# Performance work log

Measured on AMD Instinct MI355X. Metric: run time of the kernel, lower is better.

## Reference

```python
import jax, jax.numpy as jnp
import numpy as np

B, L, P, A = 32, 512, 128, 128   # batch, prot seq len, prot dim, atom dim
N = 1024                          # total atoms (32 per molecule)
H1, H2 = 512, 256                 # hidden_list


def setup_inputs() -> dict:
    key = jax.random.key(0)
    ks = jax.random.split(key, 12)
    atom_embed = jax.random.normal(ks[0], (N, A), dtype=jnp.float32)
    protSeq_embed = jax.random.normal(ks[1], (B, L, P), dtype=jnp.float32)
    # sorted segment ids, every segment non-empty (32 atoms per molecule)
    atom_splits = jnp.repeat(jnp.arange(B, dtype=jnp.int64), N // B)
    s = 0.05
    att1_W = jax.random.normal(ks[2], (P + A, 128), dtype=jnp.float32) * s
    att1_b = jnp.zeros((128,), dtype=jnp.float32)
    att2_W = jax.random.normal(ks[3], (128, 1), dtype=jnp.float32) * s
    att2_b = jnp.zeros((1,), dtype=jnp.float32)
    d1_W = jax.random.normal(ks[4], (A + P, H1), dtype=jnp.float32) * s
    d1_b = jnp.zeros((H1,), dtype=jnp.float32)
    d2_W = jax.random.normal(ks[5], (H1, H2), dtype=jnp.float32) * s
    d2_b = jnp.zeros((H2,), dtype=jnp.float32)
    out_W = jax.random.normal(ks[6], (H2, 1), dtype=jnp.float32) * s
    out_b = jnp.zeros((1,), dtype=jnp.float32)
    return {"atom_embed": atom_embed, "protSeq_embed": protSeq_embed,
            "atom_splits": atom_splits,
            "att1_W": att1_W, "att1_b": att1_b, "att2_W": att2_W, "att2_b": att2_b,
            "d1_W": d1_W, "d1_b": d1_b, "d2_W": d2_W, "d2_b": d2_b,
            "out_W": out_W, "out_b": out_b}


def reference(atom_embed, protSeq_embed, atom_splits,
              att1_W, att1_b, att2_W, att2_b,
              d1_W, d1_b, d2_W, d2_b, out_W, out_b):
    num_seg = protSeq_embed.shape[0]
    # gather protein rows per atom: [N, L, P]
    prot_g = protSeq_embed[atom_splits]
    # concat with broadcast atom embed: [N, L, P+A]
    atom_x = jnp.broadcast_to(atom_embed[:, None, :], prot_g.shape[:2] + atom_embed.shape[-1:])
    concat = jnp.concatenate([prot_g, atom_x], axis=-1)
    # attention MLP -> scores W: [N, L]
    hid = jnp.tanh(concat @ att1_W + att1_b)
    W = 5.0 * jnp.tanh(hid @ att2_W + att2_b)[..., 0]
    # atom-side weights: exp(max over seq), normalized per segment
    Wc = jnp.exp(jnp.max(W, axis=-1, keepdims=True))                     # [N, 1]
    Sc = jax.ops.segment_sum(Wc, atom_splits, num_segments=num_seg)[atom_splits]
    aa = Wc / Sc                                                          # [N, 1]
    atom_pool = jax.ops.segment_sum(aa * atom_embed, atom_splits, num_segments=num_seg)  # [B, A]
    # protein-side: segment-max scores, softmax over seq, weighted sum
    Wp = jax.ops.segment_max(W, atom_splits, num_segments=num_seg)       # [B, L]
    ap = jax.nn.softmax(Wp, axis=-1)
    prot_pool = jnp.einsum('bl,bld->bd', ap, protSeq_embed)              # [B, P]
    z = jnp.concatenate([atom_pool, prot_pool], axis=-1)
    z = jax.nn.relu(z @ d1_W + d1_b)
    z = jax.nn.relu(z @ d2_W + d2_b)
    return z @ out_W + out_b                                             # [B, 1]
```

## Files before the change

### kernel.cpp

```cpp
#include <hip/hip_runtime.h>
#include <math.h>

#define NATOMS 1024
#define BSEG   32
#define LSEQ   512

__device__ __forceinline__ float fast_tanh(float x) {
    x = fminf(fmaxf(x, -20.0f), 20.0f);
    float e = __expf(2.0f * x);
    return __fdividef(e - 1.0f, e + 1.0f);
}

__global__ __launch_bounds__(256) void row_gemm128_exp(
    const float* __restrict__ X, const float* __restrict__ Wm,
    const float* __restrict__ bias, float* __restrict__ out, int has_bias)
{
    __shared__ float x_s[16][128];
    const int tid = threadIdx.x;
    const long base = (long)blockIdx.x * 16 * 128;
    #pragma unroll
    for (int t = 0; t < 8; ++t) {
        int idx = tid + 256 * t;
        x_s[idx >> 7][idx & 127] = X[base + idx];
    }
    __syncthreads();
    const int j = tid & 127, h = tid >> 7;
    float bv = has_bias ? bias[j] : 0.0f;
    float acc[8];
    #pragma unroll
    for (int i = 0; i < 8; ++i) acc[i] = bv;
    #pragma unroll 4
    for (int k = 0; k < 128; ++k) {
        float w = Wm[k * 128 + j];
        #pragma unroll
        for (int i = 0; i < 8; ++i) acc[i] += x_s[h * 8 + i][k] * w;
    }
    #pragma unroll
    for (int i = 0; i < 8; ++i) {
        float v = fminf(fmaxf(acc[i], -20.0f), 20.0f);
        out[base + (h * 8 + i) * 128 + j] = __expf(2.0f * v);
    }
}

__global__ __launch_bounds__(256) void score2_kernel(
    const float* __restrict__ ep, const float* __restrict__ eb,
    const float* __restrict__ att2_W, const float* __restrict__ att2_b,
    float* __restrict__ Wp, float* __restrict__ pmax)
{
    __shared__ float eps[16 * 128];
    __shared__ float ebs[32 * 132];
    __shared__ float c_s[128];
    __shared__ float pm_s[8 * 33];
    __shared__ float w2sum_s;
    const int tid = threadIdx.x;
    const int chunk = blockIdx.x, b = blockIdx.y;
    const int lbase = chunk * 16;

    #pragma unroll
    for (int t = 0; t < 8; ++t) {
        int idx = tid + 256 * t;
        eps[idx] = ep[((long)b * LSEQ + lbase) * 128 + idx];
    }
    #pragma unroll
    for (int t = 0; t < 16; ++t) {
        int idx = tid + 256 * t;
        int n = idx >> 7, j = idx & 127;
        ebs[n * 132 + j] = eb[(b * 32 + n) * 128 + j];
    }
    if (tid < 128) c_s[tid] = -2.0f * att2_W[tid];
    __syncthreads();
    if (tid < 64) {
        float s = c_s[tid] + c_s[tid + 64];
        #pragma unroll
        for (int m = 32; m; m >>= 1) s += __shfl_xor(s, m);
        if (tid == 0) w2sum_s = -0.5f * s;
    }
    const float b2 = att2_b[0];
    __syncthreads();

    const int n = tid & 31, lg = tid >> 5;
    const float* ebrow = &ebs[n * 132];
    const float* ep0 = &eps[lg * 128];
    const float* ep1 = &eps[(lg + 8) * 128];
    float acc0 = 0.0f, acc1 = 0.0f;
    #pragma unroll 4
    for (int jj = 0; jj < 128; jj += 4) {
        float4 bv = *(const float4*)(ebrow + jj);
        float4 e0 = *(const float4*)(ep0 + jj);
        float4 e1 = *(const float4*)(ep1 + jj);
        float4 cv = *(const float4*)(c_s + jj);
        acc0 += cv.x * __builtin_amdgcn_rcpf(1.0f + e0.x * bv.x);
        acc1 += cv.x * __builtin_amdgcn_rcpf(1.0f + e1.x * bv.x);
        acc0 += cv.y * __builtin_amdgcn_rcpf(1.0f + e0.y * bv.y);
        acc1 += cv.y * __builtin_amdgcn_rcpf(1.0f + e1.y * bv.y);
        acc0 += cv.z * __builtin_amdgcn_rcpf(1.0f + e0.z * bv.z);
        acc1 += cv.z * __builtin_amdgcn_rcpf(1.0f + e1.z * bv.z);
        acc0 += cv.w * __builtin_amdgcn_rcpf(1.0f + e0.w * bv.w);
        acc1 += cv.w * __builtin_amdgcn_rcpf(1.0f + e1.w * bv.w);
    }
    const float base = w2sum_s + b2;
    float W0 = 5.0f * fast_tanh(acc0 + base);
    float W1 = 5.0f * fast_tanh(acc1 + base);

    float m0 = W0, m1 = W1;
    #pragma unroll
    for (int m = 16; m; m >>= 1) {
        m0 = fmaxf(m0, __shfl_xor(m0, m));
        m1 = fmaxf(m1, __shfl_xor(m1, m));
    }
    if (n == 0) {
        Wp[b * LSEQ + lbase + lg] = m0;
        Wp[b * LSEQ + lbase + lg + 8] = m1;
    }
    pm_s[lg * 33 + n] = fmaxf(W0, W1);
    __syncthreads();
    if (tid < 32) {
        float m = pm_s[tid];
        #pragma unroll
        for (int g = 1; g < 8; ++g) m = fmaxf(m, pm_s[g * 33 + tid]);
        pmax[b * 1024 + chunk * 32 + tid] = m;
    }
}

__global__ __launch_bounds__(256) void finish_kernel(
    const float* __restrict__ pmax, const float* __restrict__ Wp,
    const float* __restrict__ atom_embed, const float* __restrict__ out_b,
    float* __restrict__ ap, float* __restrict__ z, float* __restrict__ out)
{
    __shared__ float pm_s[8 * 33];
    __shared__ float expw_s[32];
    __shared__ float red[256];
    __shared__ float sinv_s;
    const int tid = threadIdx.x, b = blockIdx.x;

    {
        int n = tid & 31, cg = tid >> 5;
        float m = -1e30f;
        #pragma unroll
        for (int i = 0; i < 4; ++i)
            m = fmaxf(m, pmax[b * 1024 + (cg * 4 + i) * 32 + n]);
        pm_s[cg * 33 + n] = m;
    }
    __syncthreads();
    if (tid < 32) {
        float m = pm_s[tid];
        #pragma unroll
        for (int g = 1; g < 8; ++g) m = fmaxf(m, pm_s[g * 33 + tid]);
        expw_s[tid] = __expf(m);
    }
    __syncthreads();
    if (tid == 0) {
        float s = 0.0f;
        #pragma unroll
        for (int i = 0; i < 32; ++i) s += expw_s[i];
        sinv_s = 1.0f / s;
        out[b] = out_b[0];
    }
    __syncthreads();
    if (tid < 128) {
        float acc = 0.0f;
        #pragma unroll 4
        for (int nn = 0; nn < 32; ++nn)
            acc += expw_s[nn] * atom_embed[(b * 32 + nn) * 128 + tid];
        z[b * 256 + tid] = acc * sinv_s;
    } else {
        z[b * 256 + tid] = 0.0f;
    }
    float w0 = Wp[b * 512 + tid], w1 = Wp[b * 512 + 256 + tid];
    red[tid] = fmaxf(w0, w1);
    __syncthreads();
    for (int s = 128; s; s >>= 1) {
        if (tid < s) red[tid] = fmaxf(red[tid], red[tid + s]);
        __syncthreads();
    }
    float M = red[0];
    __syncthreads();
    float e0 = __expf(w0 - M), e1 = __expf(w1 - M);
    red[tid] = e0 + e1;
    __syncthreads();
    for (int s = 128; s; s >>= 1) {
        if (tid < s) red[tid] += red[tid + s];
        __syncthreads();
    }
    float Sinv = 1.0f / red[0];
    ap[b * 512 + tid] = e0 * Sinv;
    ap[b * 512 + 256 + tid] = e1 * Sinv;
}

__global__ __launch_bounds__(128) void prot_pool_kernel(
    const float* __restrict__ ap, const float* __restrict__ protSeq,
    float* __restrict__ z)
{
    __shared__ float ap_s[64];
    const int tid = threadIdx.x;
    const int l0 = blockIdx.x * 64, b = blockIdx.y;
    if (tid < 64) ap_s[tid] = ap[b * 512 + l0 + tid];
    __syncthreads();
    float acc = 0.0f;
    #pragma unroll 8
    for (int i = 0; i < 64; ++i)
        acc += ap_s[i] * protSeq[((long)(b * 512 + l0 + i)) * 128 + tid];
    atomicAdd(&z[b * 256 + 128 + tid], acc);
}

__global__ __launch_bounds__(256) void mlp1_kernel(
    const float* __restrict__ z, const float* __restrict__ d1_W,
    const float* __restrict__ d1_b, float* __restrict__ h1)
{
    __shared__ float zs[256];
    __shared__ float part[4 * 65];
    const int tid = threadIdx.x;
    const int c0 = blockIdx.x * 64, b = blockIdx.y;
    zs[tid] = z[b * 256 + tid];
    __syncthreads();
    const int ci = tid & 63, kg = tid >> 6;
    float acc = 0.0f;
    #pragma unroll 8
    for (int k = kg * 64; k < kg * 64 + 64; ++k)
        acc += zs[k] * d1_W[k * 512 + c0 + ci];
    part[kg * 65 + ci] = acc;
    __syncthreads();
    if (tid < 64) {
        float s = part[tid] + part[65 + tid] + part[130 + tid] + part[195 + tid]
                + d1_b[c0 + tid];
        h1[b * 512 + c0 + tid] = fmaxf(s, 0.0f);
    }
}

__global__ __launch_bounds__(256) void mlp2_kernel(
    const float* __restrict__ h1, const float* __restrict__ d2_W,
    const float* __restrict__ d2_b, const float* __restrict__ out_W,
    float* __restrict__ out)
{
    __shared__ float hs[512];
    __shared__ float part[8 * 33];
    const int tid = threadIdx.x;
    const int c0 = blockIdx.x * 32, b = blockIdx.y;
    hs[tid] = h1[b * 512 + tid];
    hs[tid + 256] = h1[b * 512 + 256 + tid];
    __syncthreads();
    const int ci = tid & 31, kg = tid >> 5;
    float acc = 0.0f;
    #pragma unroll 8
    for (int k = kg * 64; k < kg * 64 + 64; ++k)
        acc += hs[k] * d2_W[k * 256 + c0 + ci];
    part[kg * 33 + ci] = acc;
    __syncthreads();
    if (tid < 32) {
        float s = d2_b[c0 + tid];
        #pragma unroll
        for (int g = 0; g < 8; ++g) s += part[g * 33 + tid];
        float contrib = fmaxf(s, 0.0f) * out_W[c0 + tid];
        #pragma unroll
        for (int m = 16; m; m >>= 1) contrib += __shfl_xor(contrib, m);
        if (tid == 0) atomicAdd(&out[b], contrib);
    }
}

extern "C" void kernel_launch(void* const* d_in, const int* in_sizes, int n_in,
                              void* d_out, int out_size, void* d_ws, size_t ws_size,
                              hipStream_t stream) {
    const float* atom_embed = (const float*)d_in[0];
    const float* protSeq    = (const float*)d_in[1];
    const float* att1_W = (const float*)d_in[3];
    const float* att1_b = (const float*)d_in[4];
    const float* att2_W = (const float*)d_in[5];
    const float* att2_b = (const float*)d_in[6];
    const float* d1_W   = (const float*)d_in[7];
    const float* d1_b   = (const float*)d_in[8];
    const float* d2_W   = (const float*)d_in[9];
    const float* d2_b   = (const float*)d_in[10];
    const float* out_W  = (const float*)d_in[11];
    const float* out_b  = (const float*)d_in[12];
    float* out = (float*)d_out;

    float* ws = (float*)d_ws;
    float* ep   = ws;
    float* eb   = ep + 2097152;
    float* Wp   = eb + 131072;
    float* pmax = Wp + 16384;
    float* ap   = pmax + 32768;
    float* z    = ap + 16384;
    float* h1   = z + 8192;

    row_gemm128_exp<<<NATOMS / 16, 256, 0, stream>>>(atom_embed, att1_W + 128 * 128,
                                                     nullptr, eb, 0);
    row_gemm128_exp<<<(BSEG * LSEQ) / 16, 256, 0, stream>>>(protSeq, att1_W,
                                                            att1_b, ep, 1);
    score2_kernel<<<dim3(LSEQ / 16, BSEG), 256, 0, stream>>>(ep, eb, att2_W,
                                                             att2_b, Wp, pmax);
    finish_kernel<<<BSEG, 256, 0, stream>>>(pmax, Wp, atom_embed, out_b, ap, z, out);
    prot_pool_kernel<<<dim3(8, BSEG), 128, 0, stream>>>(ap, protSeq, z);
    mlp1_kernel<<<dim3(8, BSEG), 256, 0, stream>>>(z, d1_W, d1_b, h1);
    mlp2_kernel<<<dim3(8, BSEG), 256, 0, stream>>>(h1, d2_W, d2_b, out_W, out);
}
```

Before: 141.5 us.

## Merge att1 GEMMs into register-tiled kernel and fold softmax normalization into MLP

Result: faster. 128.9 us (-9.0%).

```diff
diff --git a/kernel.cpp b/kernel.cpp
--- a/kernel.cpp
+++ b/kernel.cpp
@@ -11,41 +11,81 @@
     return __fdividef(e - 1.0f, e + 1.0f);
 }
 
-__global__ __launch_bounds__(256) void row_gemm128_exp(
-    const float* __restrict__ X, const float* __restrict__ Wm,
-    const float* __restrict__ bias, float* __restrict__ out, int has_bias)
-{
-    __shared__ float x_s[16][128];
-    const int tid = threadIdx.x;
-    const long base = (long)blockIdx.x * 16 * 128;
-    #pragma unroll
-    for (int t = 0; t < 8; ++t) {
-        int idx = tid + 256 * t;
-        x_s[idx >> 7][idx & 127] = X[base + idx];
-    }
-    __syncthreads();
-    const int j = tid & 127, h = tid >> 7;
-    float bv = has_bias ? bias[j] : 0.0f;
-    float acc[8];
-    #pragma unroll
-    for (int i = 0; i < 8; ++i) acc[i] = bv;
-    #pragma unroll 4
-    for (int k = 0; k < 128; ++k) {
-        float w = Wm[k * 128 + j];
-        #pragma unroll
-        for (int i = 0; i < 8; ++i) acc[i] += x_s[h * 8 + i][k] * w;
-    }
-    #pragma unroll
-    for (int i = 0; i < 8; ++i) {
-        float v = fminf(fmaxf(acc[i], -20.0f), 20.0f);
-        out[base + (h * 8 + i) * 128 + j] = __expf(2.0f * v);
+__global__ __launch_bounds__(256) void gemm_exp_kernel(
+    const float* __restrict__ protSeq, const float* __restrict__ atom_embed,
+    const float* __restrict__ att1_W, const float* __restrict__ att1_b,
+    float* __restrict__ ep, float* __restrict__ eb)
+{
+    __shared__ float xT[64 * 68];
+    __shared__ float ws[64 * 68];
+    const int tid = threadIdx.x;
+    const int bx = blockIdx.x;
+
+    const float* Xb; const float* Wb; const float* bb; float* outp;
+    int rt, ct;
+    if (bx < 512) { rt = bx >> 1; ct = bx & 1;
+        Xb = protSeq + (long)rt * 64 * 128; Wb = att1_W; bb = att1_b;
+        outp = ep + (long)rt * 64 * 128;
+    } else { int e = bx - 512; rt = e >> 1; ct = e & 1;
+        Xb = atom_embed + (long)rt * 64 * 128; Wb = att1_W + 128 * 128; bb = nullptr;
+        outp = eb + (long)rt * 64 * 128;
+    }
+    const int c0 = ct * 64;
+    const int tx = tid & 15, ty = tid >> 4;
+
+    float acc[4][4];
+    #pragma unroll
+    for (int i = 0; i < 4; ++i)
+        #pragma unroll
+        for (int j = 0; j < 4; ++j) acc[i][j] = 0.0f;
+
+    #pragma unroll
+    for (int half = 0; half < 2; ++half) {
+        if (half) __syncthreads();
+        #pragma unroll
+        for (int i = 0; i < 16; ++i) {
+            int idx = tid + 256 * i;
+            int r = idx >> 6, kk = idx & 63;
+            xT[kk * 68 + r] = Xb[r * 128 + half * 64 + kk];
+        }
+        #pragma unroll
+        for (int i = 0; i < 16; ++i) {
+            int idx = tid + 256 * i;
+            int kk = idx >> 6, c = idx & 63;
+            ws[kk * 68 + c] = Wb[(half * 64 + kk) * 128 + c0 + c];
+        }
+        __syncthreads();
+        #pragma unroll 8
+        for (int kk = 0; kk < 64; ++kk) {
+            float4 a = *(const float4*)&xT[kk * 68 + 4 * ty];
+            float4 b = *(const float4*)&ws[kk * 68 + 4 * tx];
+            acc[0][0] += a.x * b.x; acc[0][1] += a.x * b.y;
+            acc[0][2] += a.x * b.z; acc[0][3] += a.x * b.w;
+            acc[1][0] += a.y * b.x; acc[1][1] += a.y * b.y;
+            acc[1][2] += a.y * b.z; acc[1][3] += a.y * b.w;
+            acc[2][0] += a.z * b.x; acc[2][1] += a.z * b.y;
+            acc[2][2] += a.z * b.z; acc[2][3] += a.z * b.w;
+            acc[3][0] += a.w * b.x; acc[3][1] += a.w * b.y;
+            acc[3][2] += a.w * b.z; acc[3][3] += a.w * b.w;
+        }
+    }
+    float4 bias4 = make_float4(0.f, 0.f, 0.f, 0.f);
+    if (bb) bias4 = *(const float4*)&bb[c0 + 4 * tx];
+    #pragma unroll
+    for (int i = 0; i < 4; ++i) {
+        float4 v;
+        v.x = __expf(2.0f * fminf(fmaxf(acc[i][0] + bias4.x, -20.0f), 20.0f));
+        v.y = __expf(2.0f * fminf(fmaxf(acc[i][1] + bias4.y, -20.0f), 20.0f));
+        v.z = __expf(2.0f * fminf(fmaxf(acc[i][2] + bias4.z, -20.0f), 20.0f));
+        v.w = __expf(2.0f * fminf(fmaxf(acc[i][3] + bias4.w, -20.0f), 20.0f));
+        *(float4*)&outp[(4 * ty + i) * 128 + c0 + 4 * tx] = v;
     }
 }
 
 __global__ __launch_bounds__(256) void score2_kernel(
     const float* __restrict__ ep, const float* __restrict__ eb,
     const float* __restrict__ att2_W, const float* __restrict__ att2_b,
-    float* __restrict__ Wp, float* __restrict__ pmax)
+    float* __restrict__ Wp, float* __restrict__ pmax, float* __restrict__ zr)
 {
     __shared__ float eps[16 * 128];
     __shared__ float ebs[32 * 132];
@@ -55,6 +95,8 @@
     const int tid = threadIdx.x;
     const int chunk = blockIdx.x, b = blockIdx.y;
     const int lbase = chunk * 16;
+
+    if (chunk == 0 && tid < 128) zr[b * 128 + tid] = 0.0f;
 
     #pragma unroll
     for (int t = 0; t < 8; ++t) {
@@ -122,96 +164,87 @@
     }
 }
 
-__global__ __launch_bounds__(256) void finish_kernel(
-    const float* __restrict__ pmax, const float* __restrict__ Wp,
-    const float* __restrict__ atom_embed, const float* __restrict__ out_b,
-    float* __restrict__ ap, float* __restrict__ z, float* __restrict__ out)
-{
-    __shared__ float pm_s[8 * 33];
-    __shared__ float expw_s[32];
-    __shared__ float red[256];
-    __shared__ float sinv_s;
-    const int tid = threadIdx.x, b = blockIdx.x;
-
-    {
-        int n = tid & 31, cg = tid >> 5;
-        float m = -1e30f;
-        #pragma unroll
-        for (int i = 0; i < 4; ++i)
-            m = fmaxf(m, pmax[b * 1024 + (cg * 4 + i) * 32 + n]);
-        pm_s[cg * 33 + n] = m;
-    }
-    __syncthreads();
-    if (tid < 32) {
-        float m = pm_s[tid];
-        #pragma unroll
-        for (int g = 1; g < 8; ++g) m = fmaxf(m, pm_s[g * 33 + tid]);
-        expw_s[tid] = __expf(m);
-    }
-    __syncthreads();
-    if (tid == 0) {
-        float s = 0.0f;
-        #pragma unroll
-        for (int i = 0; i < 32; ++i) s += expw_s[i];
-        sinv_s = 1.0f / s;
-        out[b] = out_b[0];
-    }
-    __syncthreads();
-    if (tid < 128) {
+__global__ __launch_bounds__(256) void tail_kernel(
+    const float* __restrict__ Wp, const float* __restrict__ pmax,
+    const float* __restrict__ atom_embed, const float* __restrict__ protSeq,
+    const float* __restrict__ out_b,
+    float* __restrict__ za, float* __restrict__ zr, float* __restrict__ dp,
+    float* __restrict__ out)
+{
+    const int tid = threadIdx.x;
+    const int bx = blockIdx.x, b = blockIdx.y;
+    if (bx < 8) {
+        __shared__ float e_s[64];
+        const int l0 = bx * 64;
+        if (tid < 64) e_s[tid] = __expf(Wp[b * 512 + l0 + tid]);
+        __syncthreads();
+        const int d = tid & 127, half = tid >> 7;
         float acc = 0.0f;
-        #pragma unroll 4
-        for (int nn = 0; nn < 32; ++nn)
-            acc += expw_s[nn] * atom_embed[(b * 32 + nn) * 128 + tid];
-        z[b * 256 + tid] = acc * sinv_s;
+        #pragma unroll 8
+        for (int i = 0; i < 32; ++i) {
+            int l = l0 + half * 32 + i;
+            acc += e_s[half * 32 + i] * protSeq[((long)(b * 512 + l)) * 128 + d];
+        }
+        atomicAdd(&zr[b * 128 + d], acc);
     } else {
-        z[b * 256 + tid] = 0.0f;
-    }
-    float w0 = Wp[b * 512 + tid], w1 = Wp[b * 512 + 256 + tid];
-    red[tid] = fmaxf(w0, w1);
-    __syncthreads();
-    for (int s = 128; s; s >>= 1) {
-        if (tid < s) red[tid] = fmaxf(red[tid], red[tid + s]);
-        __syncthreads();
-    }
-    float M = red[0];
-    __syncthreads();
-    float e0 = __expf(w0 - M), e1 = __expf(w1 - M);
-    red[tid] = e0 + e1;
-    __syncthreads();
-    for (int s = 128; s; s >>= 1) {
-        if (tid < s) red[tid] += red[tid + s];
-        __syncthreads();
-    }
-    float Sinv = 1.0f / red[0];
-    ap[b * 512 + tid] = e0 * Sinv;
-    ap[b * 512 + 256 + tid] = e1 * Sinv;
-}
-
-__global__ __launch_bounds__(128) void prot_pool_kernel(
-    const float* __restrict__ ap, const float* __restrict__ protSeq,
-    float* __restrict__ z)
-{
-    __shared__ float ap_s[64];
-    const int tid = threadIdx.x;
-    const int l0 = blockIdx.x * 64, b = blockIdx.y;
-    if (tid < 64) ap_s[tid] = ap[b * 512 + l0 + tid];
-    __syncthreads();
-    float acc = 0.0f;
-    #pragma unroll 8
-    for (int i = 0; i < 64; ++i)
-        acc += ap_s[i] * protSeq[((long)(b * 512 + l0 + i)) * 128 + tid];
-    atomicAdd(&z[b * 256 + 128 + tid], acc);
+        __shared__ float pm_s[8 * 33];
+        __shared__ float expw_s[32];
+        __shared__ float red[256];
+        __shared__ float sinv_s;
+        {
+            int n = tid & 31, cg = tid >> 5;
+            float m = -1e30f;
+            #pragma unroll
+            for (int i = 0; i < 4; ++i)
+                m = fmaxf(m, pmax[b * 1024 + (cg * 4 + i) * 32 + n]);
+            pm_s[cg * 33 + n] = m;
+        }
+        __syncthreads();
+        if (tid < 32) {
+            float m = pm_s[tid];
+            #pragma unroll
+            for (int g = 1; g < 8; ++g) m = fmaxf(m, pm_s[g * 33 + tid]);
+            expw_s[tid] = __expf(m);
+        }
+        __syncthreads();
+        if (tid == 0) {
+            float s = 0.0f;
+            #pragma unroll
+            for (int i = 0; i < 32; ++i) s += expw_s[i];
+            sinv_s = 1.0f / s;
+            out[b] = out_b[0];
+        }
+        __syncthreads();
+        if (tid < 128) {
+            float acc = 0.0f;
+            #pragma unroll 4
+            for (int nn = 0; nn < 32; ++nn)
+                acc += expw_s[nn] * atom_embed[(b * 32 + nn) * 128 + tid];
+            za[b * 128 + tid] = acc * sinv_s;
+        }
+        float e0 = __expf(Wp[b * 512 + tid]);
+        float e1 = __expf(Wp[b * 512 + 256 + tid]);
+        red[tid] = e0 + e1;
+        __syncthreads();
+        for (int s = 128; s; s >>= 1) {
+            if (tid < s) red[tid] += red[tid + s];
+            __syncthreads();
+        }
+        if (tid == 0) dp[b] = red[0];
+    }
 }
 
 __global__ __launch_bounds__(256) void mlp1_kernel(
-    const float* __restrict__ z, const float* __restrict__ d1_W,
+    const float* __restrict__ za, const float* __restrict__ zr,
+    const float* __restrict__ dp, const float* __restrict__ d1_W,
     const float* __restrict__ d1_b, float* __restrict__ h1)
 {
     __shared__ float zs[256];
     __shared__ float part[4 * 65];
     const int tid = threadIdx.x;
     const int c0 = blockIdx.x * 64, b = blockIdx.y;
-    zs[tid] = z[b * 256 + tid];
+    const float rdp = 1.0f / dp[b];
+    zs[tid] = (tid < 128) ? za[b * 128 + tid] : zr[b * 128 + tid - 128] * rdp;
     __syncthreads();
     const int ci = tid & 63, kg = tid >> 6;
     float acc = 0.0f;
@@ -279,18 +312,17 @@
     float* eb   = ep + 2097152;
     float* Wp   = eb + 131072;
     float* pmax = Wp + 16384;
-    float* ap   = pmax + 32768;
-    float* z    = ap + 16384;
-    float* h1   = z + 8192;
-
-    row_gemm128_exp<<<NATOMS / 16, 256, 0, stream>>>(atom_embed, att1_W + 128 * 128,
-                                                     nullptr, eb, 0);
-    row_gemm128_exp<<<(BSEG * LSEQ) / 16, 256, 0, stream>>>(protSeq, att1_W,
-                                                            att1_b, ep, 1);
+    float* za   = pmax + 32768;
+    float* zr   = za + 4096;
+    float* dp   = zr + 4096;
+    float* h1   = dp + 32;
+
+    gemm_exp_kernel<<<544, 256, 0, stream>>>(protSeq, atom_embed, att1_W,
+                                             att1_b, ep, eb);
     score2_kernel<<<dim3(LSEQ / 16, BSEG), 256, 0, stream>>>(ep, eb, att2_W,
-                                                             att2_b, Wp, pmax);
-    finish_kernel<<<BSEG, 256, 0, stream>>>(pmax, Wp, atom_embed, out_b, ap, z, out);
-    prot_pool_kernel<<<dim3(8, BSEG), 128, 0, stream>>>(ap, protSeq, z);
-    mlp1_kernel<<<dim3(8, BSEG), 256, 0, stream>>>(z, d1_W, d1_b, h1);
+                                                             att2_b, Wp, pmax, zr);
+    tail_kernel<<<dim3(9, BSEG), 256, 0, stream>>>(Wp, pmax, atom_embed, protSeq,
+                                                   out_b, za, zr, dp, out);
+    mlp1_kernel<<<dim3(8, BSEG), 256, 0, stream>>>(za, zr, dp, d1_W, d1_b, h1);
     mlp2_kernel<<<dim3(8, BSEG), 256, 0, stream>>>(h1, d2_W, d2_b, out_W, out);
 }
```

## Fuse pipeline into four kernels with register-tiled GEMM and fused softmax pooling

Applied to the files above, without the earlier changes.

Measured after the change: 127.1 us. 1.11x faster.

```diff
diff --git a/kernel.cpp b/kernel.cpp
--- a/kernel.cpp
+++ b/kernel.cpp
@@ -11,209 +11,242 @@
     return __fdividef(e - 1.0f, e + 1.0f);
 }
 
-__global__ __launch_bounds__(256) void row_gemm128_exp(
-    const float* __restrict__ X, const float* __restrict__ Wm,
-    const float* __restrict__ bias, float* __restrict__ out, int has_bias)
+__device__ __forceinline__ float trm(float c, float p, float e) {
+    return c * __builtin_amdgcn_rcpf(fmaf(p, e, 1.0f));
+}
+
+__global__ __launch_bounds__(256) void gemm_exp_kernel(
+    const float* __restrict__ protSeq, const float* __restrict__ atom_embed,
+    const float* __restrict__ att1_W, const float* __restrict__ att1_b,
+    float* __restrict__ ep, float* __restrict__ eb,
+    float* __restrict__ zr, float* __restrict__ dp)
 {
-    __shared__ float x_s[16][128];
-    const int tid = threadIdx.x;
-    const long base = (long)blockIdx.x * 16 * 128;
-    #pragma unroll
-    for (int t = 0; t < 8; ++t) {
-        int idx = tid + 256 * t;
-        x_s[idx >> 7][idx & 127] = X[base + idx];
-    }
-    __syncthreads();
-    const int j = tid & 127, h = tid >> 7;
-    float bv = has_bias ? bias[j] : 0.0f;
-    float acc[8];
-    #pragma unroll
-    for (int i = 0; i < 8; ++i) acc[i] = bv;
-    #pragma unroll 4
-    for (int k = 0; k < 128; ++k) {
-        float w = Wm[k * 128 + j];
-        #pragma unroll
-        for (int i = 0; i < 8; ++i) acc[i] += x_s[h * 8 + i][k] * w;
-    }
-    #pragma unroll
-    for (int i = 0; i < 8; ++i) {
-        float v = fminf(fmaxf(acc[i], -20.0f), 20.0f);
-        out[base + (h * 8 + i) * 128 + j] = __expf(2.0f * v);
-    }
-}
-
-__global__ __launch_bounds__(256) void score2_kernel(
+    __shared__ float xT[64 * 68];
+    __shared__ float wsb[64 * 132];
+    const int tid = threadIdx.x, bx = blockIdx.x;
+
+    const float* Xb; const float* Wb; const float* bb; float* outp;
+    if (bx < 256) {
+        Xb = protSeq + (long)bx * 64 * 128; Wb = att1_W; bb = att1_b;
+        outp = ep + (long)bx * 64 * 128;
+    } else {
+        int e = bx - 256;
+        zr[e * 256 + tid] = 0.0f;
+        if (e == 0 && tid < 32) dp[tid] = 0.0f;
+        Xb = atom_embed + (long)e * 64 * 128; Wb = att1_W + 128 * 128; bb = nullptr;
+        outp = eb + (long)e * 64 * 128;
+    }
+    const int tx = tid & 15, ty = tid >> 4;
+
+    float acc[4][8];
+    #pragma unroll
+    for (int i = 0; i < 4; ++i)
+        #pragma unroll
+        for (int j = 0; j < 8; ++j) acc[i][j] = 0.0f;
+
+    #pragma unroll
+    for (int half = 0; half < 2; ++half) {
+        if (half) __syncthreads();
+        #pragma unroll
+        for (int t = 0; t < 4; ++t) {
+            int flat = (tid + 256 * t) * 4;
+            int r = flat >> 6, kk = flat & 63;
+            float4 v = *(const float4*)&Xb[r * 128 + half * 64 + kk];
+            xT[kk * 68 + r] = v.x; xT[(kk + 1) * 68 + r] = v.y;
+            xT[(kk + 2) * 68 + r] = v.z; xT[(kk + 3) * 68 + r] = v.w;
+        }
+        #pragma unroll
+        for (int t = 0; t < 8; ++t) {
+            int flat = (tid + 256 * t) * 4;
+            int kk = flat >> 7, c = flat & 127;
+            *(float4*)&wsb[kk * 132 + c] = *(const float4*)&Wb[(half * 64 + kk) * 128 + c];
+        }
+        __syncthreads();
+        #pragma unroll 4
+        for (int kk = 0; kk < 64; ++kk) {
+            float4 a  = *(const float4*)&xT[kk * 68 + 4 * ty];
+            float4 w0 = *(const float4*)&wsb[kk * 132 + 8 * tx];
+            float4 w1 = *(const float4*)&wsb[kk * 132 + 8 * tx + 4];
+            #pragma unroll
+            for (int i = 0; i < 4; ++i) {
+                float av = (i == 0) ? a.x : (i == 1) ? a.y : (i == 2) ? a.z : a.w;
+                acc[i][0] += av * w0.x; acc[i][1] += av * w0.y;
+                acc[i][2] += av * w0.z; acc[i][3] += av * w0.w;
+                acc[i][4] += av * w1.x; acc[i][5] += av * w1.y;
+                acc[i][6] += av * w1.z; acc[i][7] += av * w1.w;
+            }
+        }
+    }
+    float bias[8];
+    #pragma unroll
+    for (int j = 0; j < 8; ++j) bias[j] = 0.0f;
+    if (bb) {
+        *(float4*)&bias[0] = *(const float4*)&bb[8 * tx];
+        *(float4*)&bias[4] = *(const float4*)&bb[8 * tx + 4];
+    }
+    #pragma unroll
+    for (int i = 0; i < 4; ++i) {
+        float o[8];
+        #pragma unroll
+        for (int j = 0; j < 8; ++j) {
+            float v = fminf(fmaxf(acc[i][j] + bias[j], -20.0f), 20.0f);
+            o[j] = __expf(2.0f * v);
+        }
+        int row = 4 * ty + i;
+        *(float4*)&outp[row * 128 + 8 * tx]     = make_float4(o[0], o[1], o[2], o[3]);
+        *(float4*)&outp[row * 128 + 8 * tx + 4] = make_float4(o[4], o[5], o[6], o[7]);
+    }
+}
+
+__global__ __launch_bounds__(256) void score3_kernel(
     const float* __restrict__ ep, const float* __restrict__ eb,
     const float* __restrict__ att2_W, const float* __restrict__ att2_b,
-    float* __restrict__ Wp, float* __restrict__ pmax)
+    const float* __restrict__ protSeq,
+    float* __restrict__ pmax, float* __restrict__ zr, float* __restrict__ dp)
 {
-    __shared__ float eps[16 * 128];
+    __shared__ float eps[64 * 132];
     __shared__ float ebs[32 * 132];
     __shared__ float c_s[128];
-    __shared__ float pm_s[8 * 33];
-    __shared__ float w2sum_s;
+    __shared__ float wps[64];
+    __shared__ float es[64];
+    __shared__ float pmn[32 * 33];
+    __shared__ float part[256];
+    __shared__ float base_s;
     const int tid = threadIdx.x;
     const int chunk = blockIdx.x, b = blockIdx.y;
-    const int lbase = chunk * 16;
+    const int lbase = chunk * 64;
 
     #pragma unroll
     for (int t = 0; t < 8; ++t) {
-        int idx = tid + 256 * t;
-        eps[idx] = ep[((long)b * LSEQ + lbase) * 128 + idx];
-    }
-    #pragma unroll
-    for (int t = 0; t < 16; ++t) {
-        int idx = tid + 256 * t;
-        int n = idx >> 7, j = idx & 127;
-        ebs[n * 132 + j] = eb[(b * 32 + n) * 128 + j];
+        int flat = (tid + 256 * t) * 4;
+        int l = flat >> 7, j = flat & 127;
+        *(float4*)&eps[l * 132 + j] =
+            *(const float4*)&ep[((long)(b * 512 + lbase + l)) * 128 + j];
+    }
+    #pragma unroll
+    for (int t = 0; t < 4; ++t) {
+        int flat = (tid + 256 * t) * 4;
+        int n = flat >> 7, j = flat & 127;
+        *(float4*)&ebs[n * 132 + j] = *(const float4*)&eb[(b * 32 + n) * 128 + j];
     }
     if (tid < 128) c_s[tid] = -2.0f * att2_W[tid];
     __syncthreads();
     if (tid < 64) {
         float s = c_s[tid] + c_s[tid + 64];
         #pragma unroll
-        for (int m = 32; m; m >>= 1) s += __shfl_xor(s, m);
-        if (tid == 0) w2sum_s = -0.5f * s;
-    }
-    const float b2 = att2_b[0];
-    __syncthreads();
-
-    const int n = tid & 31, lg = tid >> 5;
-    const float* ebrow = &ebs[n * 132];
-    const float* ep0 = &eps[lg * 128];
-    const float* ep1 = &eps[(lg + 8) * 128];
-    float acc0 = 0.0f, acc1 = 0.0f;
+        for (int m = 1; m < 64; m <<= 1) s += __shfl_xor(s, m);
+        if (tid == 0) base_s = -0.5f * s + att2_b[0];
+    }
+    __syncthreads();
+
+    const int ng = tid & 7, lg = tid >> 3;
+    const float* e0 = &ebs[ng * 132];
+    const float* e1 = &ebs[(ng + 8) * 132];
+    const float* e2 = &ebs[(ng + 16) * 132];
+    const float* e3 = &ebs[(ng + 24) * 132];
+    const float* p0 = &eps[lg * 132];
+    const float* p1 = &eps[(lg + 32) * 132];
+    float a00 = 0, a01 = 0, a10 = 0, a11 = 0, a20 = 0, a21 = 0, a30 = 0, a31 = 0;
+    #pragma unroll 2
+    for (int jj = 0; jj < 128; jj += 4) {
+        float4 c4 = *(const float4*)&c_s[jj];
+        float4 q0 = *(const float4*)(p0 + jj);
+        float4 q1 = *(const float4*)(p1 + jj);
+        float4 b0 = *(const float4*)(e0 + jj);
+        float4 b1 = *(const float4*)(e1 + jj);
+        float4 b2v = *(const float4*)(e2 + jj);
+        float4 b3 = *(const float4*)(e3 + jj);
+#define DOCOMP(C, Q0, Q1, B0, B1, B2, B3) \
+        a00 += trm(C, Q0, B0); a01 += trm(C, Q1, B0); \
+        a10 += trm(C, Q0, B1); a11 += trm(C, Q1, B1); \
+        a20 += trm(C, Q0, B2); a21 += trm(C, Q1, B2); \
+        a30 += trm(C, Q0, B3); a31 += trm(C, Q1, B3);
+        DOCOMP(c4.x, q0.x, q1.x, b0.x, b1.x, b2v.x, b3.x)
+        DOCOMP(c4.y, q0.y, q1.y, b0.y, b1.y, b2v.y, b3.y)
+        DOCOMP(c4.z, q0.z, q1.z, b0.z, b1.z, b2v.z, b3.z)
+        DOCOMP(c4.w, q0.w, q1.w, b0.w, b1.w, b2v.w, b3.w)
+#undef DOCOMP
+    }
+    const float bs = base_s;
+    float W00 = 5.0f * fast_tanh(a00 + bs), W01 = 5.0f * fast_tanh(a01 + bs);
+    float W10 = 5.0f * fast_tanh(a10 + bs), W11 = 5.0f * fast_tanh(a11 + bs);
+    float W20 = 5.0f * fast_tanh(a20 + bs), W21 = 5.0f * fast_tanh(a21 + bs);
+    float W30 = 5.0f * fast_tanh(a30 + bs), W31 = 5.0f * fast_tanh(a31 + bs);
+
+    float m0 = fmaxf(fmaxf(W00, W10), fmaxf(W20, W30));
+    float m1 = fmaxf(fmaxf(W01, W11), fmaxf(W21, W31));
+    #pragma unroll
+    for (int d = 1; d < 8; d <<= 1) {
+        m0 = fmaxf(m0, __shfl_xor(m0, d));
+        m1 = fmaxf(m1, __shfl_xor(m1, d));
+    }
+    if (ng == 0) { wps[lg] = m0; wps[lg + 32] = m1; }
+    pmn[lg * 33 + ng]      = fmaxf(W00, W01);
+    pmn[lg * 33 + ng + 8]  = fmaxf(W10, W11);
+    pmn[lg * 33 + ng + 16] = fmaxf(W20, W21);
+    pmn[lg * 33 + ng + 24] = fmaxf(W30, W31);
+    __syncthreads();
+    if (tid < 32) {
+        float m = pmn[tid];
+        #pragma unroll
+        for (int g = 1; g < 32; ++g) m = fmaxf(m, pmn[g * 33 + tid]);
+        pmax[b * 256 + chunk * 32 + tid] = m;
+    }
+    if (tid < 64) es[tid] = __expf(wps[tid]);
+    __syncthreads();
+    if (tid < 64) {
+        float v = es[tid];
+        #pragma unroll
+        for (int d = 1; d < 64; d <<= 1) v += __shfl_xor(v, d);
+        if (tid == 0) atomicAdd(&dp[b], v);
+    }
+    const int dd = tid & 127, hf = tid >> 7;
+    float az = 0.0f;
     #pragma unroll 4
-    for (int jj = 0; jj < 128; jj += 4) {
-        float4 bv = *(const float4*)(ebrow + jj);
-        float4 e0 = *(const float4*)(ep0 + jj);
-        float4 e1 = *(const float4*)(ep1 + jj);
-        float4 cv = *(const float4*)(c_s + jj);
-        acc0 += cv.x * __builtin_amdgcn_rcpf(1.0f + e0.x * bv.x);
-        acc1 += cv.x * __builtin_amdgcn_rcpf(1.0f + e1.x * bv.x);
-        acc0 += cv.y * __builtin_amdgcn_rcpf(1.0f + e0.y * bv.y);
-        acc1 += cv.y * __builtin_amdgcn_rcpf(1.0f + e1.y * bv.y);
-        acc0 += cv.z * __builtin_amdgcn_rcpf(1.0f + e0.z * bv.z);
-        acc1 += cv.z * __builtin_amdgcn_rcpf(1.0f + e1.z * bv.z);
-        acc0 += cv.w * __builtin_amdgcn_rcpf(1.0f + e0.w * bv.w);
-        acc1 += cv.w * __builtin_amdgcn_rcpf(1.0f + e1.w * bv.w);
-    }
-    const float base = w2sum_s + b2;
-    float W0 = 5.0f * fast_tanh(acc0 + base);
-    float W1 = 5.0f * fast_tanh(acc1 + base);
-
-    float m0 = W0, m1 = W1;
-    #pragma unroll
-    for (int m = 16; m; m >>= 1) {
-        m0 = fmaxf(m0, __shfl_xor(m0, m));
-        m1 = fmaxf(m1, __shfl_xor(m1, m));
-    }
-    if (n == 0) {
-        Wp[b * LSEQ + lbase + lg] = m0;
-        Wp[b * LSEQ + lbase + lg + 8] = m1;
-    }
-    pm_s[lg * 33 + n] = fmaxf(W0, W1);
-    __syncthreads();
-    if (tid < 32) {
-        float m = pm_s[tid];
-        #pragma unroll
-        for (int g = 1; g < 8; ++g) m = fmaxf(m, pm_s[g * 33 + tid]);
-        pmax[b * 1024 + chunk * 32 + tid] = m;
-    }
-}
-
-__global__ __launch_bounds__(256) void finish_kernel(
-    const float* __restrict__ pmax, const float* __restrict__ Wp,
-    const float* __restrict__ atom_embed, const float* __restrict__ out_b,
-    float* __restrict__ ap, float* __restrict__ z, float* __restrict__ out)
-{
-    __shared__ float pm_s[8 * 33];
-    __shared__ float expw_s[32];
-    __shared__ float red[256];
-    __shared__ float sinv_s;
-    const int tid = threadIdx.x, b = blockIdx.x;
-
-    {
-        int n = tid & 31, cg = tid >> 5;
-        float m = -1e30f;
-        #pragma unroll
-        for (int i = 0; i < 4; ++i)
-            m = fmaxf(m, pmax[b * 1024 + (cg * 4 + i) * 32 + n]);
-        pm_s[cg * 33 + n] = m;
-    }
-    __syncthreads();
-    if (tid < 32) {
-        float m = pm_s[tid];
-        #pragma unroll
-        for (int g = 1; g < 8; ++g) m = fmaxf(m, pm_s[g * 33 + tid]);
-        expw_s[tid] = __expf(m);
-    }
-    __syncthreads();
-    if (tid == 0) {
-        float s = 0.0f;
-        #pragma unroll
-        for (int i = 0; i < 32; ++i) s += expw_s[i];
-        sinv_s = 1.0f / s;
-        out[b] = out_b[0];
-    }
-    __syncthreads();
-    if (tid < 128) {
-        float acc = 0.0f;
-        #pragma unroll 4
-        for (int nn = 0; nn < 32; ++nn)
-            acc += expw_s[nn] * atom_embed[(b * 32 + nn) * 128 + tid];
-        z[b * 256 + tid] = acc * sinv_s;
-    } else {
-        z[b * 256 + tid] = 0.0f;
-    }
-    float w0 = Wp[b * 512 + tid], w1 = Wp[b * 512 + 256 + tid];
-    red[tid] = fmaxf(w0, w1);
-    __syncthreads();
-    for (int s = 128; s; s >>= 1) {
-        if (tid < s) red[tid] = fmaxf(red[tid], red[tid + s]);
-        __syncthreads();
-    }
-    float M = red[0];
-    __syncthreads();
-    float e0 = __expf(w0 - M), e1 = __expf(w1 - M);
-    red[tid] = e0 + e1;
-    __syncthreads();
-    for (int s = 128; s; s >>= 1) {
-        if (tid < s) red[tid] += red[tid + s];
-        __syncthreads();
-    }
-    float Sinv = 1.0f / red[0];
-    ap[b * 512 + tid] = e0 * Sinv;
-    ap[b * 512 + 256 + tid] = e1 * Sinv;
-}
-
-__global__ __launch_bounds__(128) void prot_pool_kernel(
-    const float* __restrict__ ap, const float* __restrict__ protSeq,
-    float* __restrict__ z)
-{
-    __shared__ float ap_s[64];
-    const int tid = threadIdx.x;
-    const int l0 = blockIdx.x * 64, b = blockIdx.y;
-    if (tid < 64) ap_s[tid] = ap[b * 512 + l0 + tid];
-    __syncthreads();
-    float acc = 0.0f;
-    #pragma unroll 8
-    for (int i = 0; i < 64; ++i)
-        acc += ap_s[i] * protSeq[((long)(b * 512 + l0 + i)) * 128 + tid];
-    atomicAdd(&z[b * 256 + 128 + tid], acc);
+    for (int i = 0; i < 32; ++i)
+        az += es[hf * 32 + i] *
+              protSeq[((long)(b * 512 + lbase + hf * 32 + i)) * 128 + dd];
+    part[tid] = az;
+    __syncthreads();
+    if (tid < 128) atomicAdd(&zr[b * 128 + tid], part[tid] + part[128 + tid]);
 }
 
 __global__ __launch_bounds__(256) void mlp1_kernel(
-    const float* __restrict__ z, const float* __restrict__ d1_W,
-    const float* __restrict__ d1_b, float* __restrict__ h1)
+    const float* __restrict__ pmax, const float* __restrict__ atom_embed,
+    const float* __restrict__ zr, const float* __restrict__ dp,
+    const float* __restrict__ d1_W, const float* __restrict__ d1_b,
+    const float* __restrict__ out_b, float* __restrict__ h1,
+    float* __restrict__ out)
 {
     __shared__ float zs[256];
     __shared__ float part[4 * 65];
+    __shared__ float expw[32];
+    __shared__ float sinv_s;
     const int tid = threadIdx.x;
-    const int c0 = blockIdx.x * 64, b = blockIdx.y;
-    zs[tid] = z[b * 256 + tid];
-    __syncthreads();
-    const int ci = tid & 63, kg = tid >> 6;
+    const int cx = blockIdx.x, b = blockIdx.y;
+    if (tid < 32) {
+        float m = -1e30f;
+        #pragma unroll
+        for (int c = 0; c < 8; ++c) m = fmaxf(m, pmax[b * 256 + c * 32 + tid]);
+        float e = __expf(m);
+        expw[tid] = e;
+        #pragma unroll
+        for (int d = 1; d < 32; d <<= 1) e += __shfl_xor(e, d);
+        if (tid == 0) sinv_s = 1.0f / e;
+    }
+    if (cx == 0 && tid == 0) out[b] = out_b[0];
+    __syncthreads();
+    if (tid < 128) {
+        float a = 0.0f;
+        #pragma unroll 4
+        for (int n = 0; n < 32; ++n)
+            a += expw[n] * atom_embed[(b * 32 + n) * 128 + tid];
+        zs[tid] = a * sinv_s;
+    } else {
+        zs[tid] = zr[b * 128 + tid - 128] * (1.0f / dp[b]);
+    }
+    __syncthreads();
+    const int c0 = cx * 64, ci = tid & 63, kg = tid >> 6;
     float acc = 0.0f;
     #pragma unroll 8
     for (int k = kg * 64; k < kg * 64 + 64; ++k)
@@ -277,20 +310,16 @@
     float* ws = (float*)d_ws;
     float* ep   = ws;
     float* eb   = ep + 2097152;
-    float* Wp   = eb + 131072;
-    float* pmax = Wp + 16384;
-    float* ap   = pmax + 32768;
-    float* z    = ap + 16384;
-    float* h1   = z + 8192;
-
-    row_gemm128_exp<<<NATOMS / 16, 256, 0, stream>>>(atom_embed, att1_W + 128 * 128,
-                                                     nullptr, eb, 0);
-    row_gemm128_exp<<<(BSEG * LSEQ) / 16, 256, 0, stream>>>(protSeq, att1_W,
-                                                            att1_b, ep, 1);
-    score2_kernel<<<dim3(LSEQ / 16, BSEG), 256, 0, stream>>>(ep, eb, att2_W,
-                                                             att2_b, Wp, pmax);
-    finish_kernel<<<BSEG, 256, 0, stream>>>(pmax, Wp, atom_embed, out_b, ap, z, out);
-    prot_pool_kernel<<<dim3(8, BSEG), 128, 0, stream>>>(ap, protSeq, z);
-    mlp1_kernel<<<dim3(8, BSEG), 256, 0, stream>>>(z, d1_W, d1_b, h1);
+    float* pmax = eb + 131072;
+    float* zr   = pmax + 8192;
+    float* dp   = zr + 4096;
+    float* h1   = dp + 32;
+
+    gemm_exp_kernel<<<272, 256, 0, stream>>>(protSeq, atom_embed, att1_W,
+                                             att1_b, ep, eb, zr, dp);
+    score3_kernel<<<dim3(8, BSEG), 256, 0, stream>>>(ep, eb, att2_W, att2_b,
+                                                     protSeq, pmax, zr, dp);
+    mlp1_kernel<<<dim3(8, BSEG), 256, 0, stream>>>(pmax, atom_embed, zr, dp,
+                                                   d1_W, d1_b, out_b, h1, out);
     mlp2_kernel<<<dim3(8, BSEG), 256, 0, stream>>>(h1, d2_W, d2_b, out_W, out);
 }
```
